# Kernel optimization log

Hardware: AMD Instinct MI355X
Metric: run time of the kernel (lower is better)

The kernel has to match this reference:

```python
import jax, jax.numpy as jnp
import numpy as np

L, D, F, H, E, V = 16, 256, 512, 8, 12, 52000  # layers, width, FFWidth, heads, experts, vocab
B, S = 4, 512
HD = D // H
EPS = 1e-5


def _ln(x, s, b):
    m = x.mean(-1, keepdims=True)
    v = ((x - m) ** 2).mean(-1, keepdims=True)
    return (x - m) / jnp.sqrt(v + EPS) * s + b


def setup_inputs() -> dict:
    key = jax.random.key(0)
    ks = jax.random.split(key, 12)
    w = lambda k, shape: (jax.random.normal(k, shape, dtype=jnp.float32) * 0.02)
    return {
        "tokens": jax.random.randint(ks[0], (B, S), 0, V),
        "emb": w(ks[1], (V, D)),
        "Wq": w(ks[2], (L, D, D)), "bq": jnp.zeros((L, D), jnp.float32),
        "Wk": w(ks[3], (L, D, D)), "bk": jnp.zeros((L, D), jnp.float32),
        "Wv": w(ks[4], (L, D, D)), "bv": jnp.zeros((L, D), jnp.float32),
        "ln1_s": jnp.ones((L, D), jnp.float32), "ln1_b": jnp.zeros((L, D), jnp.float32),
        "ln2_s": jnp.ones((L, D), jnp.float32), "ln2_b": jnp.zeros((L, D), jnp.float32),
        "gW": w(ks[5], (L, D, E)), "gb": jnp.zeros((L, E), jnp.float32),
        "ff1W": w(ks[6], (L, E, D, F)), "ff1b": jnp.zeros((L, E, F), jnp.float32),
        "ffGW": w(ks[7], (L, E, D, F)), "ffGb": jnp.zeros((L, E, F), jnp.float32),
        "ff2W": w(ks[8], (L, E, F, D)), "ff2b": jnp.zeros((L, E, D), jnp.float32),
    }


def _forward(tokens, emb, Wq, bq, Wk, bk, Wv, bv, ln1_s, ln1_b, ln2_s, ln2_b,
             gW, gb, ff1W, ff1b, ffGW, ffGb, ff2W, ff2b):
    x = emb[tokens]  # [B,S,D]
    causal = jnp.triu(jnp.full((S, S), -jnp.inf, dtype=x.dtype), 1)

    def body(x, p):
        (wq, bq_, wk, bk_, wv, bv_, l1s, l1b, l2s, l2b,
         gw, gb_, f1w, f1b, fgw, fgb, f2w, f2b) = p
        q = (x @ wq + bq_).reshape(B, S, H, HD)
        k = (x @ wk + bk_).reshape(B, S, H, HD)
        v = (x @ wv + bv_).reshape(B, S, H, HD)
        # NOTE: original applies no 1/sqrt(d) scaling -- kept faithful
        att = jnp.einsum('bshw,bShw->bhsS', q, k) + causal
        att = jax.nn.softmax(att, axis=-1)
        o = jnp.einsum('bhsS,bShw->bshw', att, v).reshape(B, S, D)
        norm = _ln(o + x, l1s, l1b)
        # MoE: top-2 experts, outputs SUMMED (no gate weighting, per original)
        probs = jax.nn.softmax(norm @ gw + gb_, axis=-1)
        _, idx = jax.lax.top_k(probs, 2)  # [B,S,2]
        msk = jax.nn.one_hot(idx, E, dtype=norm.dtype).sum(-2)  # [B,S,E] in {0,1}
        h = jax.nn.silu(jnp.einsum('bsd,edf->bsef', norm, f1w) + f1b) \
            * (jnp.einsum('bsd,edf->bsef', norm, fgw) + fgb)
        y = jnp.einsum('bsef,efd->bsed', h, f2w) + f2b
        moe = jnp.einsum('bsed,bse->bsd', y, msk)
        return _ln(moe + norm, l2s, l2b), None

    x, _ = jax.lax.scan(body, x, (Wq, bq, Wk, bk, Wv, bv, ln1_s, ln1_b, ln2_s, ln2_b,
                                  gW, gb, ff1W, ff1b, ffGW, ffGb, ff2W, ff2b))
    return x


def reference(tokens, emb, Wq, bq, Wk, bk, Wv, bv, ln1_s, ln1_b, ln2_s, ln2_b,
              gW, gb, ff1W, ff1b, ffGW, ffGb, ff2W, ff2b):
    return _forward(tokens, emb, Wq, bq, Wk, bk, Wv, bv, ln1_s, ln1_b, ln2_s, ln2_b,
                    gW, gb, ff1W, ff1b, ffGW, ffGb, ff2W, ff2b)
```

## Files before the change

kernel.cpp:

```cpp
#include <hip/hip_runtime.h>
#include <math.h>

#define LNUM 16
#define D 256
#define FF 512
#define NH 8
#define NE 12
#define HD 32
#define BB 4
#define SS 512
#define NT 2048
#define EPS 1e-5f
#define MAXT 48
#define PADROWS 5632

typedef _Float16 f16;
typedef __attribute__((ext_vector_type(8))) _Float16 f16x8;
typedef __attribute__((ext_vector_type(4))) float f32x4;
#define MFMA(A, B, C) __builtin_amdgcn_mfma_f32_16x16x32_f16((A), (B), (C), 0, 0, 0)

__device__ inline void splitf(float x, f16& h, f16& l) {
  f16 hh = (f16)x;
  h = hh;
  l = (f16)(x - (float)hh);
}

__global__ __launch_bounds__(256) void k_embed(const int* __restrict__ tok,
                                               const float* __restrict__ emb,
                                               float* __restrict__ x,
                                               f16* __restrict__ xh, f16* __restrict__ xl) {
  int n = blockIdx.x, t = threadIdx.x;
  float val = emb[(size_t)tok[n] * D + t];
  x[(size_t)n * D + t] = val;
  f16 h, l; splitf(val, h, l);
  xh[(size_t)n * D + t] = h;
  xl[(size_t)n * D + t] = l;
}

__global__ __launch_bounds__(256) void k_qkv_mfma(
    const f16* __restrict__ xh, const f16* __restrict__ xl,
    const float* __restrict__ Wq, const float* __restrict__ bq,
    const float* __restrict__ Wk, const float* __restrict__ bk,
    const float* __restrict__ Wv, const float* __restrict__ bv,
    f16* __restrict__ qhb, f16* __restrict__ qlb,
    f16* __restrict__ khb, f16* __restrict__ klb,
    f16* __restrict__ vhb, f16* __restrict__ vlb) {
  const float* W; const float* bias; f16* outh; f16* outl;
  if (blockIdx.z == 0)      { W = Wq; bias = bq; outh = qhb; outl = qlb; }
  else if (blockIdx.z == 1) { W = Wk; bias = bk; outh = khb; outl = klb; }
  else                      { W = Wv; bias = bv; outh = vhb; outl = vlb; }
  const int row0 = blockIdx.x * 128, col0 = blockIdx.y * 64;
  __shared__ f16 Ah[128][40], Al[128][40], Bh[64][40], Bl[64][40];
  const int tid = threadIdx.x;
  const int asr = tid >> 1, asc = (tid & 1) * 16;
  const int bk2 = tid >> 3, bn = (tid & 7) * 8;
  const int lane = tid & 63, w = tid >> 6;
  const int lm = lane & 15, lg = lane >> 4, lk = lg * 8;
  f32x4 acc[2][4] = {};
  for (int k0 = 0; k0 < D; k0 += 32) {
    {
      size_t ga = (size_t)(row0 + asr) * D + k0 + asc;
      *(f16x8*)&Ah[asr][asc]     = *(const f16x8*)(xh + ga);
      *(f16x8*)&Ah[asr][asc + 8] = *(const f16x8*)(xh + ga + 8);
      *(f16x8*)&Al[asr][asc]     = *(const f16x8*)(xl + ga);
      *(f16x8*)&Al[asr][asc + 8] = *(const f16x8*)(xl + ga + 8);
      const float* bp = W + (size_t)(k0 + bk2) * D + col0 + bn;
      float4 b0 = *(const float4*)bp;
      float4 b1 = *(const float4*)(bp + 4);
      f16 bh8[8], bl8[8];
      splitf(b0.x, bh8[0], bl8[0]); splitf(b0.y, bh8[1], bl8[1]);
      splitf(b0.z, bh8[2], bl8[2]); splitf(b0.w, bh8[3], bl8[3]);
      splitf(b1.x, bh8[4], bl8[4]); splitf(b1.y, bh8[5], bl8[5]);
      splitf(b1.z, bh8[6], bl8[6]); splitf(b1.w, bh8[7], bl8[7]);
#pragma unroll
      for (int j = 0; j < 8; j++) { Bh[bn + j][bk2] = bh8[j]; Bl[bn + j][bk2] = bl8[j]; }
    }
    __syncthreads();
    f16x8 a_h[2], a_l[2];
#pragma unroll
    for (int mt = 0; mt < 2; mt++) {
      a_h[mt] = *(const f16x8*)&Ah[w * 32 + mt * 16 + lm][lk];
      a_l[mt] = *(const f16x8*)&Al[w * 32 + mt * 16 + lm][lk];
    }
#pragma unroll
    for (int nt = 0; nt < 4; nt++) {
      f16x8 b_h = *(const f16x8*)&Bh[nt * 16 + lm][lk];
      f16x8 b_l = *(const f16x8*)&Bl[nt * 16 + lm][lk];
#pragma unroll
      for (int mt = 0; mt < 2; mt++) {
        f32x4 c = acc[mt][nt];
        c = MFMA(a_h[mt], b_h, c);
        c = MFMA(a_h[mt], b_l, c);
        c = MFMA(a_l[mt], b_h, c);
        acc[mt][nt] = c;
      }
    }
    __syncthreads();
  }
#pragma unroll
  for (int mt = 0; mt < 2; mt++)
#pragma unroll
    for (int nt = 0; nt < 4; nt++) {
      int col = col0 + nt * 16 + lm;
      float bv_ = bias[col];
#pragma unroll
      for (int r = 0; r < 4; r++) {
        int row = row0 + w * 32 + mt * 16 + lg * 4 + r;
        float val = acc[mt][nt][r] + bv_;
        f16 h16, l16; splitf(val, h16, l16);
        outh[(size_t)row * D + col] = h16;
        outl[(size_t)row * D + col] = l16;
      }
    }
}

__global__ __launch_bounds__(256) void k_attn_mfma(
    const f16* __restrict__ qh, const f16* __restrict__ ql,
    const f16* __restrict__ kh, const f16* __restrict__ kl,
    const f16* __restrict__ vh, const f16* __restrict__ vl,
    float* __restrict__ o) {
  const int rt = blockIdx.x, bh = blockIdx.y;
  const int b = bh >> 3, h = bh & 7;
  const int row0 = rt * 64;
  __shared__ f16 Qh[64][40], Ql[64][40], Kh[64][40], Kl[64][40];
  __shared__ f16 Vth[32][72], Vtl[32][72];
  __shared__ f16 Ph[4][16][72], Pl[4][16][72];
  const int tid = threadIdx.x;
  const int lane = tid & 63, w = tid >> 6;
  const int lm = lane & 15, lg = lane >> 4, lk = lg * 8;
  const int sr = tid >> 2, sc = (tid & 3) * 8;
  {
    size_t gq = (size_t)(b * SS + row0 + sr) * D + h * HD + sc;
    *(f16x8*)&Qh[sr][sc] = *(const f16x8*)(qh + gq);
    *(f16x8*)&Ql[sr][sc] = *(const f16x8*)(ql + gq);
  }
  f32x4 accO[2] = {};
  float mrow[4], lsum[4];
#pragma unroll
  for (int r = 0; r < 4; r++) { mrow[r] = -1e30f; lsum[r] = 0.f; }
  for (int ct = 0; ct <= rt; ct++) {
    __syncthreads();
    {
      size_t gk = (size_t)(b * SS + ct * 64 + sr) * D + h * HD + sc;
      *(f16x8*)&Kh[sr][sc] = *(const f16x8*)(kh + gk);
      *(f16x8*)&Kl[sr][sc] = *(const f16x8*)(kl + gk);
      f16x8 hv = *(const f16x8*)(vh + gk);
      f16x8 lv = *(const f16x8*)(vl + gk);
#pragma unroll
      for (int j = 0; j < 8; j++) { Vth[sc + j][sr] = hv[j]; Vtl[sc + j][sr] = lv[j]; }
    }
    __syncthreads();
    f16x8 qfh = *(const f16x8*)&Qh[w * 16 + lm][lk];
    f16x8 qfl = *(const f16x8*)&Ql[w * 16 + lm][lk];
    f32x4 s[4];
#pragma unroll
    for (int nt = 0; nt < 4; nt++) {
      f16x8 kfh = *(const f16x8*)&Kh[nt * 16 + lm][lk];
      f16x8 kfl = *(const f16x8*)&Kl[nt * 16 + lm][lk];
      f32x4 c = {};
      c = MFMA(qfh, kfh, c);
      c = MFMA(qfh, kfl, c);
      c = MFMA(qfl, kfh, c);
      s[nt] = c;
    }
    if (ct == rt) {
#pragma unroll
      for (int nt = 0; nt < 4; nt++)
#pragma unroll
        for (int r = 0; r < 4; r++)
          if (nt * 16 + lm > w * 16 + lg * 4 + r) s[nt][r] = -1e30f;
    }
    float scal[4];
#pragma unroll
    for (int r = 0; r < 4; r++) {
      float mt2 = fmaxf(fmaxf(s[0][r], s[1][r]), fmaxf(s[2][r], s[3][r]));
      mt2 = fmaxf(mt2, __shfl_xor(mt2, 1));
      mt2 = fmaxf(mt2, __shfl_xor(mt2, 2));
      mt2 = fmaxf(mt2, __shfl_xor(mt2, 4));
      mt2 = fmaxf(mt2, __shfl_xor(mt2, 8));
      float mn = fmaxf(mrow[r], mt2);
      scal[r] = expf(mrow[r] - mn);
      mrow[r] = mn;
    }
    float rs[4] = {0.f, 0.f, 0.f, 0.f};
#pragma unroll
    for (int nt = 0; nt < 4; nt++)
#pragma unroll
      for (int r = 0; r < 4; r++) {
        float pv = expf(s[nt][r] - mrow[r]);
        rs[r] += pv;
        f16 ph16, pl16; splitf(pv, ph16, pl16);
        Ph[w][lg * 4 + r][nt * 16 + lm] = ph16;
        Pl[w][lg * 4 + r][nt * 16 + lm] = pl16;
      }
#pragma unroll
    for (int r = 0; r < 4; r++) {
      rs[r] += __shfl_xor(rs[r], 1);
      rs[r] += __shfl_xor(rs[r], 2);
      rs[r] += __shfl_xor(rs[r], 4);
      rs[r] += __shfl_xor(rs[r], 8);
      lsum[r] = lsum[r] * scal[r] + rs[r];
      accO[0][r] *= scal[r];
      accO[1][r] *= scal[r];
    }
#pragma unroll
    for (int ct2 = 0; ct2 < 2; ct2++)
#pragma unroll
      for (int ks = 0; ks < 2; ks++) {
        f16x8 pa_h = *(const f16x8*)&Ph[w][lm][ks * 32 + lk];
        f16x8 pa_l = *(const f16x8*)&Pl[w][lm][ks * 32 + lk];
        f16x8 vb_h = *(const f16x8*)&Vth[ct2 * 16 + lm][ks * 32 + lk];
        f16x8 vb_l = *(const f16x8*)&Vtl[ct2 * 16 + lm][ks * 32 + lk];
        accO[ct2] = MFMA(pa_h, vb_h, accO[ct2]);
        accO[ct2] = MFMA(pa_h, vb_l, accO[ct2]);
        accO[ct2] = MFMA(pa_l, vb_h, accO[ct2]);
      }
  }
#pragma unroll
  for (int ct2 = 0; ct2 < 2; ct2++)
#pragma unroll
    for (int r = 0; r < 4; r++) {
      int grow = row0 + w * 16 + lg * 4 + r;
      o[(size_t)(b * SS + grow) * D + h * HD + ct2 * 16 + lm] = accO[ct2][r] / lsum[r];
    }
}

__global__ __launch_bounds__(256) void k_ln1gate(
    const float* __restrict__ o, const float* __restrict__ x,
    const float* __restrict__ s1, const float* __restrict__ b1,
    const float* __restrict__ gW, const float* __restrict__ gb,
    float* __restrict__ norm, f16* __restrict__ nhb, f16* __restrict__ nlb,
    int* __restrict__ eidx) {
  const int n = blockIdx.x, t = threadIdx.x;
  __shared__ float red[256];
  __shared__ float gl[NE];
  float val = o[(size_t)n * D + t] + x[(size_t)n * D + t];
  red[t] = val; __syncthreads();
  for (int s = 128; s > 0; s >>= 1) { if (t < s) red[t] += red[t + s]; __syncthreads(); }
  float m = red[0] * (1.f / D); __syncthreads();
  float df = val - m;
  red[t] = df * df; __syncthreads();
  for (int s = 128; s > 0; s >>= 1) { if (t < s) red[t] += red[t + s]; __syncthreads(); }
  float rstd = rsqrtf(red[0] * (1.f / D) + EPS); __syncthreads();
  float nv_ = df * rstd * s1[t] + b1[t];
  norm[(size_t)n * D + t] = nv_;
  f16 h16, l16; splitf(nv_, h16, l16);
  nhb[(size_t)n * D + t] = h16;
  nlb[(size_t)n * D + t] = l16;
  red[t] = nv_; __syncthreads();
  if (t < 192) {
    int e = t >> 4, di = t & 15;
    float acc = 0.f;
#pragma unroll
    for (int j = 0; j < 16; j++) acc += red[di + 16 * j] * gW[(di + 16 * j) * NE + e];
    acc += __shfl_xor(acc, 1);
    acc += __shfl_xor(acc, 2);
    acc += __shfl_xor(acc, 4);
    acc += __shfl_xor(acc, 8);
    if (di == 0) gl[e] = acc + gb[e];
  }
  __syncthreads();
  if (t == 0) {
    int i1 = 0; float v1 = gl[0];
    for (int e = 1; e < NE; e++) if (gl[e] > v1) { v1 = gl[e]; i1 = e; }
    int i2 = -1; float v2 = -3.4e38f;
    for (int e = 0; e < NE; e++) if (e != i1 && gl[e] > v2) { v2 = gl[e]; i2 = e; }
    eidx[n * 2 + 0] = i1;
    eidx[n * 2 + 1] = i2;
  }
}

__global__ __launch_bounds__(256) void k_route(const int* __restrict__ eidx,
                                               int* __restrict__ rlist, int* __restrict__ tokpos,
                                               int* __restrict__ te, int* __restrict__ tbase,
                                               int* __restrict__ tnv) {
  __shared__ int cnt[NE], cur[NE], poff[NE];
  const int t = threadIdx.x;
  if (t < NE) { cnt[t] = 0; cur[t] = 0; }
  __syncthreads();
  for (int n = t; n < NT; n += 256) {
    atomicAdd(&cnt[eidx[n * 2 + 0]], 1);
    atomicAdd(&cnt[eidx[n * 2 + 1]], 1);
  }
  __syncthreads();
  if (t == 0) {
    int off = 0, ti = 0;
    for (int e = 0; e < NE; e++) {
      poff[e] = off;
      int ntl = (cnt[e] + 127) >> 7;
      for (int tt = 0; tt < ntl; tt++) {
        te[ti] = e; tbase[ti] = off + tt * 128;
        int rem = cnt[e] - tt * 128; tnv[ti] = rem < 128 ? rem : 128;
        ti++;
      }
      off += ntl * 128;
    }
    for (; ti < MAXT; ti++) te[ti] = -1;
  }
  __syncthreads();
  for (int n = t; n < NT; n += 256) {
#pragma unroll
    for (int s2 = 0; s2 < 2; s2++) {
      int e = eidx[n * 2 + s2];
      int pos = atomicAdd(&cur[e], 1);
      int row = poff[e] + pos;
      rlist[row] = n;
      tokpos[n * 2 + s2] = row;
    }
  }
}

__global__ __launch_bounds__(256) void k_ff1_mfma(
    const f16* __restrict__ nhb, const f16* __restrict__ nlb,
    const int* __restrict__ rlist,
    const int* __restrict__ te, const int* __restrict__ tbase, const int* __restrict__ tnv,
    const float* __restrict__ W1, const float* __restrict__ b1f,
    const float* __restrict__ Wg, const float* __restrict__ bgf,
    f16* __restrict__ hhb, f16* __restrict__ hlb) {
  const int mt0 = blockIdx.x;
  const int e = te[mt0];
  if (e < 0) return;
  const int base = tbase[mt0], nv = tnv[mt0];
  const int col0 = blockIdx.y * 64;
  const float* W1e = W1 + (size_t)e * D * FF;
  const float* Wge = Wg + (size_t)e * D * FF;
  __shared__ f16 Ah[128][40], Al[128][40];
  __shared__ f16 B1h[64][40], B1l[64][40], B2h[64][40], B2l[64][40];
  __shared__ int rows[128];
  const int tid = threadIdx.x;
  if (tid < 128) rows[tid] = (tid < nv) ? rlist[base + tid] : 0;
  __syncthreads();
  const int asr = tid >> 1, asc = (tid & 1) * 16;
  const int bk2 = tid >> 3, bn = (tid & 7) * 8;
  const int lane = tid & 63, w = tid >> 6;
  const int lm = lane & 15, lg = lane >> 4, lk = lg * 8;
  f32x4 acc1[2][4] = {}, acc2[2][4] = {};
  const int arow = rows[asr];
  for (int k0 = 0; k0 < D; k0 += 32) {
    {
      size_t ga = (size_t)arow * D + k0 + asc;
      *(f16x8*)&Ah[asr][asc]     = *(const f16x8*)(nhb + ga);
      *(f16x8*)&Ah[asr][asc + 8] = *(const f16x8*)(nhb + ga + 8);
      *(f16x8*)&Al[asr][asc]     = *(const f16x8*)(nlb + ga);
      *(f16x8*)&Al[asr][asc + 8] = *(const f16x8*)(nlb + ga + 8);
      const float* b1p = W1e + (size_t)(k0 + bk2) * FF + col0 + bn;
      const float* b2p = Wge + (size_t)(k0 + bk2) * FF + col0 + bn;
      float4 u0 = *(const float4*)b1p;
      float4 u1 = *(const float4*)(b1p + 4);
      float4 g0 = *(const float4*)b2p;
      float4 g1 = *(const float4*)(b2p + 4);
      f16 bh8[8], bl8[8], ch8[8], cl8[8];
      splitf(u0.x, bh8[0], bl8[0]); splitf(u0.y, bh8[1], bl8[1]);
      splitf(u0.z, bh8[2], bl8[2]); splitf(u0.w, bh8[3], bl8[3]);
      splitf(u1.x, bh8[4], bl8[4]); splitf(u1.y, bh8[5], bl8[5]);
      splitf(u1.z, bh8[6], bl8[6]); splitf(u1.w, bh8[7], bl8[7]);
      splitf(g0.x, ch8[0], cl8[0]); splitf(g0.y, ch8[1], cl8[1]);
      splitf(g0.z, ch8[2], cl8[2]); splitf(g0.w, ch8[3], cl8[3]);
      splitf(g1.x, ch8[4], cl8[4]); splitf(g1.y, ch8[5], cl8[5]);
      splitf(g1.z, ch8[6], cl8[6]); splitf(g1.w, ch8[7], cl8[7]);
#pragma unroll
      for (int j = 0; j < 8; j++) {
        B1h[bn + j][bk2] = bh8[j]; B1l[bn + j][bk2] = bl8[j];
        B2h[bn + j][bk2] = ch8[j]; B2l[bn + j][bk2] = cl8[j];
      }
    }
    __syncthreads();
    f16x8 a_h[2], a_l[2];
#pragma unroll
    for (int mt = 0; mt < 2; mt++) {
      a_h[mt] = *(const f16x8*)&Ah[w * 32 + mt * 16 + lm][lk];
      a_l[mt] = *(const f16x8*)&Al[w * 32 + mt * 16 + lm][lk];
    }
#pragma unroll
    for (int nt = 0; nt < 4; nt++) {
      f16x8 b_h = *(const f16x8*)&B1h[nt * 16 + lm][lk];
      f16x8 b_l = *(const f16x8*)&B1l[nt * 16 + lm][lk];
      f16x8 c_h = *(const f16x8*)&B2h[nt * 16 + lm][lk];
      f16x8 c_l = *(const f16x8*)&B2l[nt * 16 + lm][lk];
#pragma unroll
      for (int mt = 0; mt < 2; mt++) {
        f32x4 c1 = acc1[mt][nt];
        c1 = MFMA(a_h[mt], b_h, c1);
        c1 = MFMA(a_h[mt], b_l, c1);
        c1 = MFMA(a_l[mt], b_h, c1);
        acc1[mt][nt] = c1;
        f32x4 c2 = acc2[mt][nt];
        c2 = MFMA(a_h[mt], c_h, c2);
        c2 = MFMA(a_h[mt], c_l, c2);
        c2 = MFMA(a_l[mt], c_h, c2);
        acc2[mt][nt] = c2;
      }
    }
    __syncthreads();
  }
#pragma unroll
  for (int mt = 0; mt < 2; mt++)
#pragma unroll
    for (int nt = 0; nt < 4; nt++) {
      int col = col0 + nt * 16 + lm;
      float bb1 = b1f[e * FF + col], bb2 = bgf[e * FF + col];
#pragma unroll
      for (int r = 0; r < 4; r++) {
        int rit = w * 32 + mt * 16 + lg * 4 + r;
        if (rit < nv) {
          float z1 = acc1[mt][nt][r] + bb1;
          float zg = acc2[mt][nt][r] + bb2;
          float sl = z1 / (1.f + expf(-z1));
          float hv = sl * zg;
          f16 h16, l16; splitf(hv, h16, l16);
          hhb[(size_t)(base + rit) * FF + col] = h16;
          hlb[(size_t)(base + rit) * FF + col] = l16;
        }
      }
    }
}

__global__ __launch_bounds__(256) void k_ff2_mfma(
    const f16* __restrict__ hhb, const f16* __restrict__ hlb,
    const int* __restrict__ te, const int* __restrict__ tbase, const int* __restrict__ tnv,
    const float* __restrict__ W2, const float* __restrict__ b2f,
    float* __restrict__ ybuf) {
  const int mt0 = blockIdx.x;
  const int e = te[mt0];
  if (e < 0) return;
  const int base = tbase[mt0], nv = tnv[mt0];
  const int col0 = blockIdx.y * 64;
  const float* W2e = W2 + (size_t)e * FF * D;
  __shared__ f16 Ah[128][40], Al[128][40], Bh[64][40], Bl[64][40];
  const int tid = threadIdx.x;
  const int asr = tid >> 1, asc = (tid & 1) * 16;
  const int bk2 = tid >> 3, bn = (tid & 7) * 8;
  const int lane = tid & 63, w = tid >> 6;
  const int lm = lane & 15, lg = lane >> 4, lk = lg * 8;
  f32x4 acc[2][4] = {};
  for (int k0 = 0; k0 < FF; k0 += 32) {
    {
      size_t ga = (size_t)(base + asr) * FF + k0 + asc;
      *(f16x8*)&Ah[asr][asc]     = *(const f16x8*)(hhb + ga);
      *(f16x8*)&Ah[asr][asc + 8] = *(const f16x8*)(hhb + ga + 8);
      *(f16x8*)&Al[asr][asc]     = *(const f16x8*)(hlb + ga);
      *(f16x8*)&Al[asr][asc + 8] = *(const f16x8*)(hlb + ga + 8);
      const float* bp = W2e + (size_t)(k0 + bk2) * D + col0 + bn;
      float4 b0 = *(const float4*)bp;
      float4 b1 = *(const float4*)(bp + 4);
      f16 bh8[8], bl8[8];
      splitf(b0.x, bh8[0], bl8[0]); splitf(b0.y, bh8[1], bl8[1]);
      splitf(b0.z, bh8[2], bl8[2]); splitf(b0.w, bh8[3], bl8[3]);
      splitf(b1.x, bh8[4], bl8[4]); splitf(b1.y, bh8[5], bl8[5]);
      splitf(b1.z, bh8[6], bl8[6]); splitf(b1.w, bh8[7], bl8[7]);
#pragma unroll
      for (int j = 0; j < 8; j++) { Bh[bn + j][bk2] = bh8[j]; Bl[bn + j][bk2] = bl8[j]; }
    }
    __syncthreads();
    f16x8 a_h[2], a_l[2];
#pragma unroll
    for (int mt = 0; mt < 2; mt++) {
      a_h[mt] = *(const f16x8*)&Ah[w * 32 + mt * 16 + lm][lk];
      a_l[mt] = *(const f16x8*)&Al[w * 32 + mt * 16 + lm][lk];
    }
#pragma unroll
    for (int nt = 0; nt < 4; nt++) {
      f16x8 b_h = *(const f16x8*)&Bh[nt * 16 + lm][lk];
      f16x8 b_l = *(const f16x8*)&Bl[nt * 16 + lm][lk];
#pragma unroll
      for (int mt = 0; mt < 2; mt++) {
        f32x4 c = acc[mt][nt];
        c = MFMA(a_h[mt], b_h, c);
        c = MFMA(a_h[mt], b_l, c);
        c = MFMA(a_l[mt], b_h, c);
        acc[mt][nt] = c;
      }
    }
    __syncthreads();
  }
#pragma unroll
  for (int mt = 0; mt < 2; mt++)
#pragma unroll
    for (int nt = 0; nt < 4; nt++) {
      int col = col0 + nt * 16 + lm;
      float bb = b2f[e * D + col];
#pragma unroll
      for (int r = 0; r < 4; r++) {
        int rit = w * 32 + mt * 16 + lg * 4 + r;
        if (rit < nv) ybuf[(size_t)(base + rit) * D + col] = acc[mt][nt][r] + bb;
      }
    }
}

__global__ __launch_bounds__(256) void k_ln2(
    const float* __restrict__ ybuf, const int* __restrict__ tokpos,
    const float* __restrict__ norm, const float* __restrict__ s2, const float* __restrict__ b2,
    float* __restrict__ out, f16* __restrict__ xh, f16* __restrict__ xl) {
  const int n = blockIdx.x, t = threadIdx.x;
  __shared__ float red[256];
  int p0 = tokpos[n * 2 + 0], p1 = tokpos[n * 2 + 1];
  float val = ybuf[(size_t)p0 * D + t] + ybuf[(size_t)p1 * D + t] + norm[(size_t)n * D + t];
  red[t] = val; __syncthreads();
  for (int s = 128; s > 0; s >>= 1) { if (t < s) red[t] += red[t + s]; __syncthreads(); }
  float m = red[0] * (1.f / D); __syncthreads();
  float df = val - m;
  red[t] = df * df; __syncthreads();
  for (int s = 128; s > 0; s >>= 1) { if (t < s) red[t] += red[t + s]; __syncthreads(); }
  float rstd = rsqrtf(red[0] * (1.f / D) + EPS);
  float ov = df * rstd * s2[t] + b2[t];
  out[(size_t)n * D + t] = ov;
  f16 h16, l16; splitf(ov, h16, l16);
  xh[(size_t)n * D + t] = h16;
  xl[(size_t)n * D + t] = l16;
}

extern "C" void kernel_launch(void* const* d_in, const int* in_sizes, int n_in,
                              void* d_out, int out_size, void* d_ws, size_t ws_size,
                              hipStream_t stream) {
  (void)in_sizes; (void)n_in; (void)out_size; (void)ws_size;
  const int*   tok = (const int*)d_in[0];
  const float* emb = (const float*)d_in[1];
  const float* Wq  = (const float*)d_in[2];
  const float* bq  = (const float*)d_in[3];
  const float* Wk  = (const float*)d_in[4];
  const float* bk  = (const float*)d_in[5];
  const float* Wv  = (const float*)d_in[6];
  const float* bv  = (const float*)d_in[7];
  const float* l1s = (const float*)d_in[8];
  const float* l1b = (const float*)d_in[9];
  const float* l2s = (const float*)d_in[10];
  const float* l2b = (const float*)d_in[11];
  const float* gW  = (const float*)d_in[12];
  const float* gb  = (const float*)d_in[13];
  const float* f1W = (const float*)d_in[14];
  const float* f1b = (const float*)d_in[15];
  const float* fgW = (const float*)d_in[16];
  const float* fgb = (const float*)d_in[17];
  const float* f2W = (const float*)d_in[18];
  const float* f2b = (const float*)d_in[19];
  float* out = (float*)d_out;

  char* p = (char*)d_ws;
  auto alloc = [&](size_t bytes) { char* r = p; p += (bytes + 255) & ~(size_t)255; return r; };
  float* xb = (float*)alloc((size_t)NT * D * 4);
  f16* xh = (f16*)alloc((size_t)NT * D * 2);
  f16* xl = (f16*)alloc((size_t)NT * D * 2);
  f16* qhb = (f16*)alloc((size_t)NT * D * 2);
  f16* qlb = (f16*)alloc((size_t)NT * D * 2);
  f16* khb = (f16*)alloc((size_t)NT * D * 2);
  f16* klb = (f16*)alloc((size_t)NT * D * 2);
  f16* vhb = (f16*)alloc((size_t)NT * D * 2);
  f16* vlb = (f16*)alloc((size_t)NT * D * 2);
  float* ob = (float*)alloc((size_t)NT * D * 4);
  float* nb = (float*)alloc((size_t)NT * D * 4);
  f16* nhb = (f16*)alloc((size_t)NT * D * 2);
  f16* nlb = (f16*)alloc((size_t)NT * D * 2);
  f16* hhb = (f16*)alloc((size_t)PADROWS * FF * 2);
  f16* hlb = (f16*)alloc((size_t)PADROWS * FF * 2);
  float* yb = (float*)alloc((size_t)PADROWS * D * 4);
  int* eidx   = (int*)alloc((size_t)NT * 2 * 4);
  int* rlist  = (int*)alloc((size_t)PADROWS * 4);
  int* tokpos = (int*)alloc((size_t)NT * 2 * 4);
  int* te     = (int*)alloc(MAXT * 4);
  int* tbase  = (int*)alloc(MAXT * 4);
  int* tnv    = (int*)alloc(MAXT * 4);

  k_embed<<<NT, 256, 0, stream>>>(tok, emb, xb, xh, xl);

  for (int l = 0; l < LNUM; l++) {
    k_qkv_mfma<<<dim3(16, 4, 3), 256, 0, stream>>>(
        xh, xl,
        Wq + (size_t)l * D * D, bq + (size_t)l * D,
        Wk + (size_t)l * D * D, bk + (size_t)l * D,
        Wv + (size_t)l * D * D, bv + (size_t)l * D,
        qhb, qlb, khb, klb, vhb, vlb);
    k_attn_mfma<<<dim3(8, 32), 256, 0, stream>>>(qhb, qlb, khb, klb, vhb, vlb, ob);
    k_ln1gate<<<NT, 256, 0, stream>>>(ob, xb, l1s + (size_t)l * D, l1b + (size_t)l * D,
                                      gW + (size_t)l * D * NE, gb + (size_t)l * NE,
                                      nb, nhb, nlb, eidx);
    k_route<<<1, 256, 0, stream>>>(eidx, rlist, tokpos, te, tbase, tnv);
    k_ff1_mfma<<<dim3(MAXT, 8), 256, 0, stream>>>(
        nhb, nlb, rlist, te, tbase, tnv,
        f1W + (size_t)l * NE * D * FF, f1b + (size_t)l * NE * FF,
        fgW + (size_t)l * NE * D * FF, fgb + (size_t)l * NE * FF, hhb, hlb);
    k_ff2_mfma<<<dim3(MAXT, 4), 256, 0, stream>>>(
        hhb, hlb, te, tbase, tnv,
        f2W + (size_t)l * NE * FF * D, f2b + (size_t)l * NE * D, yb);
    k_ln2<<<NT, 256, 0, stream>>>(yb, tokpos, nb, l2s + (size_t)l * D, l2b + (size_t)l * D,
                                  (l == LNUM - 1) ? out : xb, xh, xl);
  }
}
```

Measured before the change: 2.024 ms.

## Pre-split and transpose weights to fp16 hi/lo once; warp-per-row layernorms

Adds a prep kernel that converts every fp32 weight matrix (QKV, FF1, gate, FF2) into transposed fp16 hi/lo pairs once per call. The GEMM kernels then load weight tiles with vectorized f16x8 copies instead of converting and scattering fp32 values inside every tile loop. LDS row padding changes from 40 to 44. Separately, the LN1+gate and LN2 kernels now handle four tokens per block, one wavefront per token, using shuffle reductions instead of shared-memory tree reductions with many barriers. The prep pass rereads all ~150MB of weights and writes them back out, which is extra traffic at the start of every call. The variance is now computed as E[x²]-mean², which is slightly less numerically stable than the two-pass form.

```diff
diff --git a/kernel.cpp b/kernel.cpp
--- a/kernel.cpp
+++ b/kernel.cpp
@@ -16,6 +16,7 @@
 
 typedef _Float16 f16;
 typedef __attribute__((ext_vector_type(8))) _Float16 f16x8;
+typedef __attribute__((ext_vector_type(4))) _Float16 f16x4;
 typedef __attribute__((ext_vector_type(4))) float f32x4;
 #define MFMA(A, B, C) __builtin_amdgcn_mfma_f32_16x16x32_f16((A), (B), (C), 0, 0, 0)
 
@@ -23,6 +24,34 @@
   f16 hh = (f16)x;
   h = hh;
   l = (f16)(x - (float)hh);
+}
+
+__global__ __launch_bounds__(256) void k_wprep(const float* __restrict__ src,
+                                               f16* __restrict__ dh, f16* __restrict__ dl,
+                                               int K, int N) {
+  const size_t msz = (size_t)K * N * blockIdx.z;
+  src += msz; dh += msz; dl += msz;
+  const int n0 = blockIdx.x * 32, k0 = blockIdx.y * 32;
+  __shared__ f16 th[32][36], tl[32][36];
+  const int t = threadIdx.x;
+  {
+    const int r = t >> 3, c4 = (t & 7) * 4;
+    float4 v = *(const float4*)(src + (size_t)(k0 + r) * N + n0 + c4);
+    f16 h0, l0, h1, l1, h2, l2, h3, l3;
+    splitf(v.x, h0, l0); splitf(v.y, h1, l1);
+    splitf(v.z, h2, l2); splitf(v.w, h3, l3);
+    th[c4 + 0][r] = h0; tl[c4 + 0][r] = l0;
+    th[c4 + 1][r] = h1; tl[c4 + 1][r] = l1;
+    th[c4 + 2][r] = h2; tl[c4 + 2][r] = l2;
+    th[c4 + 3][r] = h3; tl[c4 + 3][r] = l3;
+  }
+  __syncthreads();
+  const int rn = t >> 3, ck = (t & 7) * 4;
+  f16x4 hv, lv;
+#pragma unroll
+  for (int j = 0; j < 4; j++) { hv[j] = th[rn][ck + j]; lv[j] = tl[rn][ck + j]; }
+  *(f16x4*)(dh + (size_t)(n0 + rn) * K + k0 + ck) = hv;
+  *(f16x4*)(dl + (size_t)(n0 + rn) * K + k0 + ck) = lv;
 }
 
 __global__ __launch_bounds__(256) void k_embed(const int* __restrict__ tok,
@@ -39,21 +68,21 @@
 
 __global__ __launch_bounds__(256) void k_qkv_mfma(
     const f16* __restrict__ xh, const f16* __restrict__ xl,
-    const float* __restrict__ Wq, const float* __restrict__ bq,
-    const float* __restrict__ Wk, const float* __restrict__ bk,
-    const float* __restrict__ Wv, const float* __restrict__ bv,
+    const f16* __restrict__ wqh, const f16* __restrict__ wql, const float* __restrict__ bq,
+    const f16* __restrict__ wkh, const f16* __restrict__ wkl, const float* __restrict__ bk,
+    const f16* __restrict__ wvh, const f16* __restrict__ wvl, const float* __restrict__ bv,
     f16* __restrict__ qhb, f16* __restrict__ qlb,
     f16* __restrict__ khb, f16* __restrict__ klb,
     f16* __restrict__ vhb, f16* __restrict__ vlb) {
-  const float* W; const float* bias; f16* outh; f16* outl;
-  if (blockIdx.z == 0)      { W = Wq; bias = bq; outh = qhb; outl = qlb; }
-  else if (blockIdx.z == 1) { W = Wk; bias = bk; outh = khb; outl = klb; }
-  else                      { W = Wv; bias = bv; outh = vhb; outl = vlb; }
+  const f16* Wh; const f16* Wl; const float* bias; f16* outh; f16* outl;
+  if (blockIdx.z == 0)      { Wh = wqh; Wl = wql; bias = bq; outh = qhb; outl = qlb; }
+  else if (blockIdx.z == 1) { Wh = wkh; Wl = wkl; bias = bk; outh = khb; outl = klb; }
+  else                      { Wh = wvh; Wl = wvl; bias = bv; outh = vhb; outl = vlb; }
   const int row0 = blockIdx.x * 128, col0 = blockIdx.y * 64;
-  __shared__ f16 Ah[128][40], Al[128][40], Bh[64][40], Bl[64][40];
+  __shared__ f16 Ah[128][44], Al[128][44], Bh[64][44], Bl[64][44];
   const int tid = threadIdx.x;
   const int asr = tid >> 1, asc = (tid & 1) * 16;
-  const int bk2 = tid >> 3, bn = (tid & 7) * 8;
+  const int bn2 = tid >> 2, bkc = (tid & 3) * 8;
   const int lane = tid & 63, w = tid >> 6;
   const int lm = lane & 15, lg = lane >> 4, lk = lg * 8;
   f32x4 acc[2][4] = {};
@@ -64,16 +93,9 @@
       *(f16x8*)&Ah[asr][asc + 8] = *(const f16x8*)(xh + ga + 8);
       *(f16x8*)&Al[asr][asc]     = *(const f16x8*)(xl + ga);
       *(f16x8*)&Al[asr][asc + 8] = *(const f16x8*)(xl + ga + 8);
-      const float* bp = W + (size_t)(k0 + bk2) * D + col0 + bn;
-      float4 b0 = *(const float4*)bp;
-      float4 b1 = *(const float4*)(bp + 4);
-      f16 bh8[8], bl8[8];
-      splitf(b0.x, bh8[0], bl8[0]); splitf(b0.y, bh8[1], bl8[1]);
-      splitf(b0.z, bh8[2], bl8[2]); splitf(b0.w, bh8[3], bl8[3]);
-      splitf(b1.x, bh8[4], bl8[4]); splitf(b1.y, bh8[5], bl8[5]);
-      splitf(b1.z, bh8[6], bl8[6]); splitf(b1.w, bh8[7], bl8[7]);
-#pragma unroll
-      for (int j = 0; j < 8; j++) { Bh[bn + j][bk2] = bh8[j]; Bl[bn + j][bk2] = bl8[j]; }
+      size_t gb = (size_t)(col0 + bn2) * D + k0 + bkc;
+      *(f16x8*)&Bh[bn2][bkc] = *(const f16x8*)(Wh + gb);
+      *(f16x8*)&Bl[bn2][bkc] = *(const f16x8*)(Wl + gb);
     }
     __syncthreads();
     f16x8 a_h[2], a_l[2];
@@ -231,40 +253,51 @@
     const float* __restrict__ gW, const float* __restrict__ gb,
     float* __restrict__ norm, f16* __restrict__ nhb, f16* __restrict__ nlb,
     int* __restrict__ eidx) {
-  const int n = blockIdx.x, t = threadIdx.x;
-  __shared__ float red[256];
-  __shared__ float gl[NE];
-  float val = o[(size_t)n * D + t] + x[(size_t)n * D + t];
-  red[t] = val; __syncthreads();
-  for (int s = 128; s > 0; s >>= 1) { if (t < s) red[t] += red[t + s]; __syncthreads(); }
-  float m = red[0] * (1.f / D); __syncthreads();
-  float df = val - m;
-  red[t] = df * df; __syncthreads();
-  for (int s = 128; s > 0; s >>= 1) { if (t < s) red[t] += red[t + s]; __syncthreads(); }
-  float rstd = rsqrtf(red[0] * (1.f / D) + EPS); __syncthreads();
-  float nv_ = df * rstd * s1[t] + b1[t];
-  norm[(size_t)n * D + t] = nv_;
-  f16 h16, l16; splitf(nv_, h16, l16);
-  nhb[(size_t)n * D + t] = h16;
-  nlb[(size_t)n * D + t] = l16;
-  red[t] = nv_; __syncthreads();
-  if (t < 192) {
-    int e = t >> 4, di = t & 15;
-    float acc = 0.f;
-#pragma unroll
-    for (int j = 0; j < 16; j++) acc += red[di + 16 * j] * gW[(di + 16 * j) * NE + e];
-    acc += __shfl_xor(acc, 1);
-    acc += __shfl_xor(acc, 2);
-    acc += __shfl_xor(acc, 4);
-    acc += __shfl_xor(acc, 8);
-    if (di == 0) gl[e] = acc + gb[e];
-  }
-  __syncthreads();
-  if (t == 0) {
-    int i1 = 0; float v1 = gl[0];
-    for (int e = 1; e < NE; e++) if (gl[e] > v1) { v1 = gl[e]; i1 = e; }
+  const int w = threadIdx.x >> 6, lane = threadIdx.x & 63;
+  const int n = blockIdx.x * 4 + w;
+  float val[4], s1v = 0.f, s2v = 0.f;
+#pragma unroll
+  for (int j = 0; j < 4; j++) {
+    int d = lane + 64 * j;
+    float v = o[(size_t)n * D + d] + x[(size_t)n * D + d];
+    val[j] = v; s1v += v; s2v += v * v;
+  }
+#pragma unroll
+  for (int m = 1; m < 64; m <<= 1) {
+    s1v += __shfl_xor(s1v, m);
+    s2v += __shfl_xor(s2v, m);
+  }
+  float mean = s1v * (1.f / D);
+  float var = s2v * (1.f / D) - mean * mean;
+  float rstd = rsqrtf(var + EPS);
+  float ge[NE];
+#pragma unroll
+  for (int e = 0; e < NE; e++) ge[e] = 0.f;
+#pragma unroll
+  for (int j = 0; j < 4; j++) {
+    int d = lane + 64 * j;
+    float nv = (val[j] - mean) * rstd * s1[d] + b1[d];
+    norm[(size_t)n * D + d] = nv;
+    f16 h16, l16; splitf(nv, h16, l16);
+    nhb[(size_t)n * D + d] = h16;
+    nlb[(size_t)n * D + d] = l16;
+    const float* gr = gW + (size_t)d * NE;
+#pragma unroll
+    for (int e = 0; e < NE; e++) ge[e] += nv * gr[e];
+  }
+#pragma unroll
+  for (int m = 1; m < 64; m <<= 1)
+#pragma unroll
+    for (int e = 0; e < NE; e++) ge[e] += __shfl_xor(ge[e], m);
+  if (lane == 0) {
+#pragma unroll
+    for (int e = 0; e < NE; e++) ge[e] += gb[e];
+    int i1 = 0; float v1 = ge[0];
+#pragma unroll
+    for (int e = 1; e < NE; e++) if (ge[e] > v1) { v1 = ge[e]; i1 = e; }
     int i2 = -1; float v2 = -3.4e38f;
-    for (int e = 0; e < NE; e++) if (e != i1 && gl[e] > v2) { v2 = gl[e]; i2 = e; }
+#pragma unroll
+    for (int e = 0; e < NE; e++) if (e != i1 && ge[e] > v2) { v2 = ge[e]; i2 = e; }
     eidx[n * 2 + 0] = i1;
     eidx[n * 2 + 1] = i2;
   }
@@ -314,24 +347,26 @@
     const f16* __restrict__ nhb, const f16* __restrict__ nlb,
     const int* __restrict__ rlist,
     const int* __restrict__ te, const int* __restrict__ tbase, const int* __restrict__ tnv,
-    const float* __restrict__ W1, const float* __restrict__ b1f,
-    const float* __restrict__ Wg, const float* __restrict__ bgf,
+    const f16* __restrict__ w1th, const f16* __restrict__ w1tl, const float* __restrict__ b1f,
+    const f16* __restrict__ wgth, const f16* __restrict__ wgtl, const float* __restrict__ bgf,
     f16* __restrict__ hhb, f16* __restrict__ hlb) {
   const int mt0 = blockIdx.x;
   const int e = te[mt0];
   if (e < 0) return;
   const int base = tbase[mt0], nv = tnv[mt0];
   const int col0 = blockIdx.y * 64;
-  const float* W1e = W1 + (size_t)e * D * FF;
-  const float* Wge = Wg + (size_t)e * D * FF;
-  __shared__ f16 Ah[128][40], Al[128][40];
-  __shared__ f16 B1h[64][40], B1l[64][40], B2h[64][40], B2l[64][40];
+  const f16* W1h = w1th + (size_t)e * D * FF;
+  const f16* W1l = w1tl + (size_t)e * D * FF;
+  const f16* Wgh = wgth + (size_t)e * D * FF;
+  const f16* Wgl = wgtl + (size_t)e * D * FF;
+  __shared__ f16 Ah[128][44], Al[128][44];
+  __shared__ f16 B1h[64][44], B1l[64][44], B2h[64][44], B2l[64][44];
   __shared__ int rows[128];
   const int tid = threadIdx.x;
   if (tid < 128) rows[tid] = (tid < nv) ? rlist[base + tid] : 0;
   __syncthreads();
   const int asr = tid >> 1, asc = (tid & 1) * 16;
-  const int bk2 = tid >> 3, bn = (tid & 7) * 8;
+  const int bn2 = tid >> 2, bkc = (tid & 3) * 8;
   const int lane = tid & 63, w = tid >> 6;
   const int lm = lane & 15, lg = lane >> 4, lk = lg * 8;
   f32x4 acc1[2][4] = {}, acc2[2][4] = {};
@@ -343,26 +378,11 @@
       *(f16x8*)&Ah[asr][asc + 8] = *(const f16x8*)(nhb + ga + 8);
       *(f16x8*)&Al[asr][asc]     = *(const f16x8*)(nlb + ga);
       *(f16x8*)&Al[asr][asc + 8] = *(const f16x8*)(nlb + ga + 8);
-      const float* b1p = W1e + (size_t)(k0 + bk2) * FF + col0 + bn;
-      const float* b2p = Wge + (size_t)(k0 + bk2) * FF + col0 + bn;
-      float4 u0 = *(const float4*)b1p;
-      float4 u1 = *(const float4*)(b1p + 4);
-      float4 g0 = *(const float4*)b2p;
-      float4 g1 = *(const float4*)(b2p + 4);
-      f16 bh8[8], bl8[8], ch8[8], cl8[8];
-      splitf(u0.x, bh8[0], bl8[0]); splitf(u0.y, bh8[1], bl8[1]);
-      splitf(u0.z, bh8[2], bl8[2]); splitf(u0.w, bh8[3], bl8[3]);
-      splitf(u1.x, bh8[4], bl8[4]); splitf(u1.y, bh8[5], bl8[5]);
-      splitf(u1.z, bh8[6], bl8[6]); splitf(u1.w, bh8[7], bl8[7]);
-      splitf(g0.x, ch8[0], cl8[0]); splitf(g0.y, ch8[1], cl8[1]);
-      splitf(g0.z, ch8[2], cl8[2]); splitf(g0.w, ch8[3], cl8[3]);
-      splitf(g1.x, ch8[4], cl8[4]); splitf(g1.y, ch8[5], cl8[5]);
-      splitf(g1.z, ch8[6], cl8[6]); splitf(g1.w, ch8[7], cl8[7]);
-#pragma unroll
-      for (int j = 0; j < 8; j++) {
-        B1h[bn + j][bk2] = bh8[j]; B1l[bn + j][bk2] = bl8[j];
-        B2h[bn + j][bk2] = ch8[j]; B2l[bn + j][bk2] = cl8[j];
-      }
+      size_t gb = (size_t)(col0 + bn2) * D + k0 + bkc;
+      *(f16x8*)&B1h[bn2][bkc] = *(const f16x8*)(W1h + gb);
+      *(f16x8*)&B1l[bn2][bkc] = *(const f16x8*)(W1l + gb);
+      *(f16x8*)&B2h[bn2][bkc] = *(const f16x8*)(Wgh + gb);
+      *(f16x8*)&B2l[bn2][bkc] = *(const f16x8*)(Wgl + gb);
     }
     __syncthreads();
     f16x8 a_h[2], a_l[2];
@@ -418,18 +438,19 @@
 __global__ __launch_bounds__(256) void k_ff2_mfma(
     const f16* __restrict__ hhb, const f16* __restrict__ hlb,
     const int* __restrict__ te, const int* __restrict__ tbase, const int* __restrict__ tnv,
-    const float* __restrict__ W2, const float* __restrict__ b2f,
+    const f16* __restrict__ w2th, const f16* __restrict__ w2tl, const float* __restrict__ b2f,
     float* __restrict__ ybuf) {
   const int mt0 = blockIdx.x;
   const int e = te[mt0];
   if (e < 0) return;
   const int base = tbase[mt0], nv = tnv[mt0];
   const int col0 = blockIdx.y * 64;
-  const float* W2e = W2 + (size_t)e * FF * D;
-  __shared__ f16 Ah[128][40], Al[128][40], Bh[64][40], Bl[64][40];
+  const f16* W2h = w2th + (size_t)e * FF * D;
+  const f16* W2l = w2tl + (size_t)e * FF * D;
+  __shared__ f16 Ah[128][44], Al[128][44], Bh[64][44], Bl[64][44];
   const int tid = threadIdx.x;
   const int asr = tid >> 1, asc = (tid & 1) * 16;
-  const int bk2 = tid >> 3, bn = (tid & 7) * 8;
+  const int bn2 = tid >> 2, bkc = (tid & 3) * 8;
   const int lane = tid & 63, w = tid >> 6;
   const int lm = lane & 15, lg = lane >> 4, lk = lg * 8;
   f32x4 acc[2][4] = {};
@@ -440,16 +461,9 @@
       *(f16x8*)&Ah[asr][asc + 8] = *(const f16x8*)(hhb + ga + 8);
       *(f16x8*)&Al[asr][asc]     = *(const f16x8*)(hlb + ga);
       *(f16x8*)&Al[asr][asc + 8] = *(const f16x8*)(hlb + ga + 8);
-      const float* bp = W2e + (size_t)(k0 + bk2) * D + col0 + bn;
-      float4 b0 = *(const float4*)bp;
-      float4 b1 = *(const float4*)(bp + 4);
-      f16 bh8[8], bl8[8];
-      splitf(b0.x, bh8[0], bl8[0]); splitf(b0.y, bh8[1], bl8[1]);
-      splitf(b0.z, bh8[2], bl8[2]); splitf(b0.w, bh8[3], bl8[3]);
-      splitf(b1.x, bh8[4], bl8[4]); splitf(b1.y, bh8[5], bl8[5]);
-      splitf(b1.z, bh8[6], bl8[6]); splitf(b1.w, bh8[7], bl8[7]);
-#pragma unroll
-      for (int j = 0; j < 8; j++) { Bh[bn + j][bk2] = bh8[j]; Bl[bn + j][bk2] = bl8[j]; }
+      size_t gb = (size_t)(col0 + bn2) * FF + k0 + bkc;
+      *(f16x8*)&Bh[bn2][bkc] = *(const f16x8*)(W2h + gb);
+      *(f16x8*)&Bl[bn2][bkc] = *(const f16x8*)(W2l + gb);
     }
     __syncthreads();
     f16x8 a_h[2], a_l[2];
@@ -490,23 +504,34 @@
 __global__ __launch_bounds__(256) void k_ln2(
     const float* __restrict__ ybuf, const int* __restrict__ tokpos,
     const float* __restrict__ norm, const float* __restrict__ s2, const float* __restrict__ b2,
-    float* __restrict__ out, f16* __restrict__ xh, f16* __restrict__ xl) {
-  const int n = blockIdx.x, t = threadIdx.x;
-  __shared__ float red[256];
-  int p0 = tokpos[n * 2 + 0], p1 = tokpos[n * 2 + 1];
-  float val = ybuf[(size_t)p0 * D + t] + ybuf[(size_t)p1 * D + t] + norm[(size_t)n * D + t];
-  red[t] = val; __syncthreads();
-  for (int s = 128; s > 0; s >>= 1) { if (t < s) red[t] += red[t + s]; __syncthreads(); }
-  float m = red[0] * (1.f / D); __syncthreads();
-  float df = val - m;
-  red[t] = df * df; __syncthreads();
-  for (int s = 128; s > 0; s >>= 1) { if (t < s) red[t] += red[t + s]; __syncthreads(); }
-  float rstd = rsqrtf(red[0] * (1.f / D) + EPS);
-  float ov = df * rstd * s2[t] + b2[t];
-  out[(size_t)n * D + t] = ov;
-  f16 h16, l16; splitf(ov, h16, l16);
-  xh[(size_t)n * D + t] = h16;
-  xl[(size_t)n * D + t] = l16;
+    float* __restrict__ dst, f16* __restrict__ xh, f16* __restrict__ xl) {
+  const int w = threadIdx.x >> 6, lane = threadIdx.x & 63;
+  const int n = blockIdx.x * 4 + w;
+  const int p0 = tokpos[n * 2 + 0], p1 = tokpos[n * 2 + 1];
+  float val[4], s1v = 0.f, s2v = 0.f;
+#pragma unroll
+  for (int j = 0; j < 4; j++) {
+    int d = lane + 64 * j;
+    float v = ybuf[(size_t)p0 * D + d] + ybuf[(size_t)p1 * D + d] + norm[(size_t)n * D + d];
+    val[j] = v; s1v += v; s2v += v * v;
+  }
+#pragma unroll
+  for (int m = 1; m < 64; m <<= 1) {
+    s1v += __shfl_xor(s1v, m);
+    s2v += __shfl_xor(s2v, m);
+  }
+  float mean = s1v * (1.f / D);
+  float var = s2v * (1.f / D) - mean * mean;
+  float rstd = rsqrtf(var + EPS);
+#pragma unroll
+  for (int j = 0; j < 4; j++) {
+    int d = lane + 64 * j;
+    float ov = (val[j] - mean) * rstd * s2[d] + b2[d];
+    dst[(size_t)n * D + d] = ov;
+    f16 h16, l16; splitf(ov, h16, l16);
+    xh[(size_t)n * D + d] = h16;
+    xl[(size_t)n * D + d] = l16;
+  }
 }
 
 extern "C" void kernel_launch(void* const* d_in, const int* in_sizes, int n_in,
@@ -559,29 +584,46 @@
   int* te     = (int*)alloc(MAXT * 4);
   int* tbase  = (int*)alloc(MAXT * 4);
   int* tnv    = (int*)alloc(MAXT * 4);
+  size_t qkvsz = (size_t)LNUM * D * D;
+  size_t ffsz  = (size_t)LNUM * NE * D * FF;
+  f16* wqh = (f16*)alloc(qkvsz * 2); f16* wql = (f16*)alloc(qkvsz * 2);
+  f16* wkh = (f16*)alloc(qkvsz * 2); f16* wkl = (f16*)alloc(qkvsz * 2);
+  f16* wvh = (f16*)alloc(qkvsz * 2); f16* wvl = (f16*)alloc(qkvsz * 2);
+  f16* w1th = (f16*)alloc(ffsz * 2); f16* w1tl = (f16*)alloc(ffsz * 2);
+  f16* wgth = (f16*)alloc(ffsz * 2); f16* wgtl = (f16*)alloc(ffsz * 2);
+  f16* w2th = (f16*)alloc(ffsz * 2); f16* w2tl = (f16*)alloc(ffsz * 2);
+
+  k_wprep<<<dim3(D / 32, D / 32, LNUM), 256, 0, stream>>>(Wq, wqh, wql, D, D);
+  k_wprep<<<dim3(D / 32, D / 32, LNUM), 256, 0, stream>>>(Wk, wkh, wkl, D, D);
+  k_wprep<<<dim3(D / 32, D / 32, LNUM), 256, 0, stream>>>(Wv, wvh, wvl, D, D);
+  k_wprep<<<dim3(FF / 32, D / 32, LNUM * NE), 256, 0, stream>>>(f1W, w1th, w1tl, D, FF);
+  k_wprep<<<dim3(FF / 32, D / 32, LNUM * NE), 256, 0, stream>>>(fgW, wgth, wgtl, D, FF);
+  k_wprep<<<dim3(D / 32, FF / 32, LNUM * NE), 256, 0, stream>>>(f2W, w2th, w2tl, FF, D);
 
   k_embed<<<NT, 256, 0, stream>>>(tok, emb, xb, xh, xl);
 
   for (int l = 0; l < LNUM; l++) {
     k_qkv_mfma<<<dim3(16, 4, 3), 256, 0, stream>>>(
         xh, xl,
-        Wq + (size_t)l * D * D, bq + (size_t)l * D,
-        Wk + (size_t)l * D * D, bk + (size_t)l * D,
-        Wv + (size_t)l * D * D, bv + (size_t)l * D,
+        wqh + (size_t)l * D * D, wql + (size_t)l * D * D, bq + (size_t)l * D,
+        wkh + (size_t)l * D * D, wkl + (size_t)l * D * D, bk + (size_t)l * D,
+        wvh + (size_t)l * D * D, wvl + (size_t)l * D * D, bv + (size_t)l * D,
         qhb, qlb, khb, klb, vhb, vlb);
     k_attn_mfma<<<dim3(8, 32), 256, 0, stream>>>(qhb, qlb, khb, klb, vhb, vlb, ob);
-    k_ln1gate<<<NT, 256, 0, stream>>>(ob, xb, l1s + (size_t)l * D, l1b + (size_t)l * D,
-                                      gW + (size_t)l * D * NE, gb + (size_t)l * NE,
-                                      nb, nhb, nlb, eidx);
+    k_ln1gate<<<NT / 4, 256, 0, stream>>>(ob, xb, l1s + (size_t)l * D, l1b + (size_t)l * D,
+                                          gW + (size_t)l * D * NE, gb + (size_t)l * NE,
+                                          nb, nhb, nlb, eidx);
     k_route<<<1, 256, 0, stream>>>(eidx, rlist, tokpos, te, tbase, tnv);
     k_ff1_mfma<<<dim3(MAXT, 8), 256, 0, stream>>>(
         nhb, nlb, rlist, te, tbase, tnv,
-        f1W + (size_t)l * NE * D * FF, f1b + (size_t)l * NE * FF,
-        fgW + (size_t)l * NE * D * FF, fgb + (size_t)l * NE * FF, hhb, hlb);
+        w1th + (size_t)l * NE * D * FF, w1tl + (size_t)l * NE * D * FF, f1b + (size_t)l * NE * FF,
+        wgth + (size_t)l * NE * D * FF, wgtl + (size_t)l * NE * D * FF, fgb + (size_t)l * NE * FF,
+        hhb, hlb);
     k_ff2_mfma<<<dim3(MAXT, 4), 256, 0, stream>>>(
         hhb, hlb, te, tbase, tnv,
-        f2W + (size_t)l * NE * FF * D, f2b + (size_t)l * NE * D, yb);
-    k_ln2<<<NT, 256, 0, stream>>>(yb, tokpos, nb, l2s + (size_t)l * D, l2b + (size_t)l * D,
-                                  (l == LNUM - 1) ? out : xb, xh, xl);
-  }
-}
+        w2th + (size_t)l * NE * FF * D, w2tl + (size_t)l * NE * FF * D, f2b + (size_t)l * NE * D,
+        yb);
+    k_ln2<<<NT / 4, 256, 0, stream>>>(yb, tokpos, nb, l2s + (size_t)l * D, l2b + (size_t)l * D,
+                                      (l == LNUM - 1) ? out : xb, xh, xl);
+  }
+}
```

Result: faster. 1.974 ms (-2.4%).
